# Optimization experiments

Measured on AMD Instinct MI355X. Metric: run time of the kernel, lower is better.

The kernel has to match this reference:

```python
import jax, jax.numpy as jnp
import numpy as np

B, S, D = 2, 2048, 1024
H, DH = 16, 64
IGNORE = -100000.0
ATTN_SCALE = float(np.sqrt(DH))


def setup_inputs() -> dict:
    key = jax.random.key(0)
    ks = jax.random.split(key, 9)
    sc = 0.02
    return {
        "x": jax.random.normal(ks[0], (B, S, D), dtype=jnp.float32),
        "W_Q": jax.random.normal(ks[1], (H, DH, D), dtype=jnp.float32) * sc,
        "W_K": jax.random.normal(ks[2], (H, DH, D), dtype=jnp.float32) * sc,
        "W_V": jax.random.normal(ks[3], (H, DH, D), dtype=jnp.float32) * sc,
        "W_O": jax.random.normal(ks[4], (H, D, DH), dtype=jnp.float32) * sc,
        "b_Q": jax.random.normal(ks[5], (H, DH), dtype=jnp.float32) * sc,
        "b_K": jax.random.normal(ks[6], (H, DH), dtype=jnp.float32) * sc,
        "b_V": jax.random.normal(ks[7], (H, DH), dtype=jnp.float32) * sc,
        "b_O": jax.random.normal(ks[8], (D,), dtype=jnp.float32) * sc,
    }


def reference(x, W_Q, W_K, W_V, W_O, b_Q, b_K, b_V, b_O):
    # QKV projections: [b, pos, head, d_head]
    q = jnp.einsum('ihm,bpm->bpih', W_Q, x) + b_Q
    k = jnp.einsum('ihm,bpm->bpih', W_K, x) + b_K
    v = jnp.einsum('ihm,bpm->bpih', W_V, x) + b_V
    # scores[b, head, query_pos, key_pos]
    scores = jnp.einsum('bpih,bqih->bipq', q, k) / ATTN_SCALE
    Sq = x.shape[1]
    causal = jnp.tril(jnp.ones((Sq, Sq), dtype=bool))  # global causal mask
    scores = jnp.where(causal, scores, jnp.float32(IGNORE))
    attn = jax.nn.softmax(scores, axis=-1)
    # z[b, query_pos, head, d_head]
    z = jnp.einsum('bpih,biqp->bqih', v, attn)
    out = jnp.einsum('idh,bqih->bqd', W_O, z) + b_O
    return out
```

## Files before the change

kernel.cpp:

```cpp
#include <hip/hip_runtime.h>
#include <stdint.h>

typedef __attribute__((ext_vector_type(8))) short short8;
typedef __attribute__((ext_vector_type(4))) float f32x4;

#define AS1(p) ((const __attribute__((address_space(1))) void*)(p))
#define AS3(p) ((__attribute__((address_space(3))) void*)(p))

__device__ __forceinline__ void gload_lds16(const void* g, void* l) {
  __builtin_amdgcn_global_load_lds(AS1(g), AS3(l), 16, 0, 0);
}

__device__ __forceinline__ uint32_t cvtpk_bf16(float a, float b) {
  uint32_t d;
  asm("v_cvt_pk_bf16_f32 %0, %1, %2" : "=v"(d) : "v"(a), "v"(b));
  return d;
}

__device__ __forceinline__ float fast_exp2(float x) {
#if __has_builtin(__builtin_amdgcn_exp2f)
  return __builtin_amdgcn_exp2f(x);
#else
  return exp2f(x);
#endif
}

#define QSCALE 0.1803368801111244f

__global__ void prep_k(const float* __restrict__ x, const float* __restrict__ wq,
                       const float* __restrict__ wk, const float* __restrict__ wv,
                       const float* __restrict__ wo, const float* __restrict__ bq,
                       const float* __restrict__ bk, const float* __restrict__ bv,
                       uint2* __restrict__ xb, uint2* __restrict__ wqkvb,
                       uint2* __restrict__ mob, float* __restrict__ bqkv) {
  const int bid = blockIdx.x, tid = threadIdx.x;
  if (bid < 4096) {
    int i = bid * 256 + tid;
    float4 v = ((const float4*)x)[i];
    uint2 o; o.x = cvtpk_bf16(v.x, v.y); o.y = cvtpk_bf16(v.z, v.w);
    xb[i] = o;
  } else if (bid < 7168) {
    int i = (bid - 4096) * 256 + tid;
    int e = i * 4;
    const float* src = (e < (1 << 20)) ? (wq + e)
                     : (e < (2 << 20)) ? (wk + (e - (1 << 20)))
                                       : (wv + (e - (2 << 20)));
    float4 v = *(const float4*)src;
    uint2 o; o.x = cvtpk_bf16(v.x, v.y); o.y = cvtpk_bf16(v.z, v.w);
    wqkvb[i] = o;
  } else if (bid < 8192) {
    int i = (bid - 7168) * 256 + tid;
    int o4 = i * 4;
    int d = o4 >> 10, c = o4 & 1023;
    const float* s = wo + ((c >> 6) << 16) + (d << 6) + (c & 63);
    float4 v = *(const float4*)s;
    uint2 o; o.x = cvtpk_bf16(v.x, v.y); o.y = cvtpk_bf16(v.z, v.w);
    mob[i] = o;
  } else {
    int i = (bid - 8192) * 256 + tid;
    bqkv[i] = (i < 1024) ? bq[i] : (i < 2048) ? bk[i - 1024] : bv[i - 2048];
  }
}

__global__ __launch_bounds__(256) void gemm_bt(const short* __restrict__ A,
                                               const short* __restrict__ Bm,
                                               const float* __restrict__ bias,
                                               unsigned short* __restrict__ Cout,
                                               int K, int ldc) {
  __shared__ short As[128 * 64];
  __shared__ short Bs[128 * 64];
  const int t = threadIdx.x;
  const int l = t & 63, w = t >> 6;
  const int wr = w >> 1, wc = w & 1;
  const int q = l & 15, g = l >> 4;
  const long brow = (long)blockIdx.y * 128;
  const long bcol = (long)blockIdx.x * 128;
  f32x4 acc[4][4] = {};
  const int r8 = t >> 3;
  const int sc8 = (t & 7) ^ (r8 & 7);
  const short* aptr = A + (brow + r8) * (long)K + sc8 * 8;
  const short* bptr = Bm + (bcol + r8) * (long)K + sc8 * 8;
  const int qs = q & 7;
  for (int k0 = 0; k0 < K; k0 += 64) {
#pragma unroll
    for (int c = 0; c < 4; ++c) {
      gload_lds16(aptr + k0 + c * 32 * (long)K, &As[(c * 256 + t) * 8]);
      gload_lds16(bptr + k0 + c * 32 * (long)K, &Bs[(c * 256 + t) * 8]);
    }
    __syncthreads();
    short8 af[4][2], bfr[4][2];
#pragma unroll
    for (int m = 0; m < 4; ++m)
#pragma unroll
      for (int kk = 0; kk < 2; ++kk)
        af[m][kk] = *(const short8*)&As[(wr * 64 + m * 16 + q) * 64 + ((kk * 4 + g) ^ qs) * 8];
#pragma unroll
    for (int n = 0; n < 4; ++n)
#pragma unroll
      for (int kk = 0; kk < 2; ++kk)
        bfr[n][kk] = *(const short8*)&Bs[(wc * 64 + n * 16 + q) * 64 + ((kk * 4 + g) ^ qs) * 8];
#pragma unroll
    for (int m = 0; m < 4; ++m)
#pragma unroll
      for (int n = 0; n < 4; ++n) {
        acc[m][n] = __builtin_amdgcn_mfma_f32_16x16x32_bf16(af[m][0], bfr[n][0], acc[m][n], 0, 0, 0);
        acc[m][n] = __builtin_amdgcn_mfma_f32_16x16x32_bf16(af[m][1], bfr[n][1], acc[m][n], 0, 0, 0);
      }
    if (k0 + 64 < K) __syncthreads();
  }
#pragma unroll
  for (int m = 0; m < 4; ++m)
#pragma unroll
    for (int n = 0; n < 4; ++n)
#pragma unroll
      for (int r = 0; r < 4; ++r) {
        long row = brow + wr * 64 + m * 16 + g * 4 + r;
        long col = bcol + wc * 64 + n * 16 + q;
        float v = acc[m][n][r] + bias[col];
        if (col < 1024) v *= QSCALE;
        Cout[row * ldc + col] = (unsigned short)cvtpk_bf16(v, v);
      }
}

__global__ __launch_bounds__(256) void gemm_bt2(const short* __restrict__ A,
                                                const short* __restrict__ Bm,
                                                const float* __restrict__ bias,
                                                float* __restrict__ Cout,
                                                int K, int ldc) {
  __shared__ short As[128 * 64];
  __shared__ short Bs[64 * 64];
  const int t = threadIdx.x;
  const int l = t & 63, w = t >> 6;
  const int q = l & 15, g = l >> 4;
  const long brow = (long)blockIdx.y * 128;
  const long bcol = (long)blockIdx.x * 64;
  f32x4 acc[2][4] = {};
  const int r8 = t >> 3;
  const int sc8 = (t & 7) ^ (r8 & 7);
  const short* aptr = A + (brow + r8) * (long)K + sc8 * 8;
  const short* bptr = Bm + (bcol + r8) * (long)K + sc8 * 8;
  const int qs = q & 7;
  for (int k0 = 0; k0 < K; k0 += 64) {
#pragma unroll
    for (int c = 0; c < 4; ++c)
      gload_lds16(aptr + k0 + c * 32 * (long)K, &As[(c * 256 + t) * 8]);
#pragma unroll
    for (int c = 0; c < 2; ++c)
      gload_lds16(bptr + k0 + c * 32 * (long)K, &Bs[(c * 256 + t) * 8]);
    __syncthreads();
    short8 af[2][2], bfr[4][2];
#pragma unroll
    for (int m = 0; m < 2; ++m)
#pragma unroll
      for (int kk = 0; kk < 2; ++kk)
        af[m][kk] = *(const short8*)&As[(w * 32 + m * 16 + q) * 64 + ((kk * 4 + g) ^ qs) * 8];
#pragma unroll
    for (int n = 0; n < 4; ++n)
#pragma unroll
      for (int kk = 0; kk < 2; ++kk)
        bfr[n][kk] = *(const short8*)&Bs[(n * 16 + q) * 64 + ((kk * 4 + g) ^ qs) * 8];
#pragma unroll
    for (int m = 0; m < 2; ++m)
#pragma unroll
      for (int n = 0; n < 4; ++n) {
        acc[m][n] = __builtin_amdgcn_mfma_f32_16x16x32_bf16(af[m][0], bfr[n][0], acc[m][n], 0, 0, 0);
        acc[m][n] = __builtin_amdgcn_mfma_f32_16x16x32_bf16(af[m][1], bfr[n][1], acc[m][n], 0, 0, 0);
      }
    if (k0 + 64 < K) __syncthreads();
  }
#pragma unroll
  for (int m = 0; m < 2; ++m)
#pragma unroll
    for (int n = 0; n < 4; ++n)
#pragma unroll
      for (int r = 0; r < 4; ++r) {
        long row = brow + w * 32 + m * 16 + g * 4 + r;
        long col = bcol + n * 16 + q;
        Cout[row * ldc + col] = acc[m][n][r] + bias[col];
      }
}

__global__ __launch_bounds__(256) void attn(const short* __restrict__ qkv,
                                            unsigned short* __restrict__ zb) {
  __shared__ short Ks[2][64 * 64];
  __shared__ short Vt[64 * 64];
  __shared__ unsigned short Ps[8][16 * 64];
  const int bid = blockIdx.x;
  const int r_ = bid >> 7;
  const int u_ = (bid >> 3) & 15;
  const int x_ = bid & 7;
  const int bh = r_ * 8 + x_;
  const int pr = (r_ < 2) ? u_ : 15 - u_;
  const int qtA = 31 - pr, qtB = pr;
  const int b = bh >> 4, h = bh & 15;
  const int t = threadIdx.x, l = t & 63, w = t >> 6;
  const int lq = l & 15, g = l >> 4;
  const int u = t >> 3, c8 = t & 7;
  const long rowbase = (long)b * 2048;
  const short* qp = qkv + rowbase * 3072 + h * 64;
  const short* kp = qp + 1024;
  const short* vp = qp + 2048;

  short8 qfA[2], qfB[2];
#pragma unroll
  for (int kg = 0; kg < 2; ++kg) {
    qfA[kg] = *(const short8*)(qp + (long)(qtA * 64 + w * 16 + lq) * 3072 + kg * 32 + g * 8);
    qfB[kg] = *(const short8*)(qp + (long)(qtB * 64 + w * 16 + lq) * 3072 + kg * 32 + g * 8);
  }
  f32x4 zA[4] = {}, zB[4] = {};
  float mA = -1e30f, lA = 0.0f, mB = -1e30f, lB = 0.0f;

  auto step = [&](const short* ksb, unsigned short* Pw, f32x4 (&zacc)[4],
                  float& mrun, float& lrun, short8 (&qf)[2], bool diag) {
    f32x4 sacc[4] = {};
#pragma unroll
    for (int m = 0; m < 4; ++m) {
#pragma unroll
      for (int kg = 0; kg < 2; ++kg) {
        int krow = m * 16 + lq;
        int blk = kg * 4 + g;
        short8 kf = *(const short8*)&ksb[krow * 64 + (blk ^ (krow & 7)) * 8];
        sacc[m] = __builtin_amdgcn_mfma_f32_16x16x32_bf16(kf, qf[kg], sacc[m], 0, 0, 0);
      }
    }
    if (diag) {
#pragma unroll
      for (int m = 0; m < 4; ++m)
#pragma unroll
        for (int r = 0; r < 4; ++r)
          if (m * 16 + g * 4 + r > w * 16 + lq) sacc[m][r] = -1e30f;
    }
    float red[8];
#pragma unroll
    for (int i2 = 0; i2 < 8; ++i2)
      red[i2] = fmaxf(sacc[i2 >> 2][i2 & 3], sacc[2 + (i2 >> 2)][i2 & 3]);
#pragma unroll
    for (int i2 = 0; i2 < 4; ++i2) red[i2] = fmaxf(red[i2], red[i2 + 4]);
    float mx = fmaxf(fmaxf(red[0], red[2]), fmaxf(red[1], red[3]));
    mx = fmaxf(mx, __shfl_xor(mx, 16));
    mx = fmaxf(mx, __shfl_xor(mx, 32));
    if (!__all(mx <= mrun + 8.0f)) {
      float mnew = fmaxf(mrun, mx);
      float alpha = fast_exp2(mrun - mnew);
      lrun *= alpha;
#pragma unroll
      for (int r = 0; r < 4; ++r) {
        float ar = __shfl(alpha, g * 4 + r);
#pragma unroll
        for (int n2 = 0; n2 < 4; ++n2) zacc[n2][r] *= ar;
      }
      mrun = mnew;
    }
#pragma unroll
    for (int m = 0; m < 4; ++m)
#pragma unroll
      for (int r = 0; r < 4; ++r) sacc[m][r] = fast_exp2(sacc[m][r] - mrun);
    float rs[8];
#pragma unroll
    for (int i2 = 0; i2 < 8; ++i2)
      rs[i2] = sacc[i2 >> 2][i2 & 3] + sacc[2 + (i2 >> 2)][i2 & 3];
#pragma unroll
    for (int i2 = 0; i2 < 4; ++i2) rs[i2] = rs[i2] + rs[i2 + 4];
    float ts = (rs[0] + rs[2]) + (rs[1] + rs[3]);
    ts += __shfl_xor(ts, 16);
    ts += __shfl_xor(ts, 32);
    lrun += ts;
#pragma unroll
    for (int m = 0; m < 4; ++m) {
      uint2 wv;
      wv.x = cvtpk_bf16(sacc[m][0], sacc[m][1]);
      wv.y = cvtpk_bf16(sacc[m][2], sacc[m][3]);
      int c = m * 4 + g;
      int csw = c ^ ((lq & 7) << 1);
      *(uint2*)&Pw[lq * 64 + csw * 4] = wv;
    }
    short8 pf[2];
#pragma unroll
    for (int kg2 = 0; kg2 < 2; ++kg2) {
      int c0 = kg2 * 8 + g * 2;
      int c0s = c0 ^ ((lq & 7) << 1);
      pf[kg2] = *(const short8*)&Pw[lq * 64 + c0s * 4];
    }
#pragma unroll
    for (int n2 = 0; n2 < 4; ++n2) {
#pragma unroll
      for (int kg2 = 0; kg2 < 2; ++kg2) {
        int dh = n2 * 16 + lq;
        int sw = (dh & 7) ^ ((dh >> 3) & 7);
        int blk = kg2 * 4 + g;
        short8 vf = *(const short8*)&Vt[dh * 64 + ((blk ^ sw) * 8)];
        zacc[n2] = __builtin_amdgcn_mfma_f32_16x16x32_bf16(pf[kg2], vf, zacc[n2], 0, 0, 0);
      }
    }
  };

  auto stageK = [&](int tile, int buf) {
#pragma unroll
    for (int i = 0; i < 2; ++i) {
      int r = i * 32 + u;
      int cbk = (c8 ^ (r & 7)) * 8;
      gload_lds16(kp + (long)(tile * 64 + r) * 3072 + cbk, &Ks[buf][i * 2048 + t * 8]);
    }
  };

  short8 va0, va1;
  {
    stageK(0, 0);
    const short* vrow = vp + (long)(2 * u) * 3072 + c8 * 8;
    va0 = *(const short8*)vrow;
    va1 = *(const short8*)(vrow + 3072);
  }

  for (int j = 0; j <= qtA; ++j) {
    const int buf = j & 1;
    asm volatile("s_waitcnt vmcnt(0)" ::: "memory");
    __builtin_amdgcn_sched_barrier(0);
    __builtin_amdgcn_s_barrier();
    {
      int blk = u >> 2, rl = (u & 3) * 2;
#pragma unroll
      for (int idx = 0; idx < 8; ++idx) {
        int dh = c8 * 8 + idx;
        int sw = (dh & 7) ^ ((dh >> 3) & 7);
        uint32_t pk = (uint32_t)(uint16_t)va0[idx] | ((uint32_t)(uint16_t)va1[idx] << 16);
        *(uint32_t*)&Vt[dh * 64 + ((blk ^ sw) * 8) + rl] = pk;
      }
    }
    if (j < qtA) {
      stageK(j + 1, buf ^ 1);
      const short* vrow = vp + (long)((j + 1) * 64 + 2 * u) * 3072 + c8 * 8;
      va0 = *(const short8*)vrow;
      va1 = *(const short8*)(vrow + 3072);
    }
    asm volatile("s_waitcnt lgkmcnt(0)" ::: "memory");
    __builtin_amdgcn_sched_barrier(0);
    __builtin_amdgcn_s_barrier();
    step(&Ks[buf][0], &Ps[w][0], zA, mA, lA, qfA, j == qtA);
    if (j <= qtB)
      step(&Ks[buf][0], &Ps[4 + w][0], zB, mB, lB, qfB, j == qtB);
  }

  auto wout = [&](f32x4 (&zacc)[4], float lrun, int qt) {
#pragma unroll
    for (int r = 0; r < 4; ++r) {
      float linv = 1.0f / __shfl(lrun, g * 4 + r);
      long grow = rowbase + qt * 64 + w * 16 + g * 4 + r;
#pragma unroll
      for (int n2 = 0; n2 < 4; ++n2) {
        int col = h * 64 + n2 * 16 + lq;
        float zv = zacc[n2][r] * linv;
        zb[grow * 1024 + col] = (unsigned short)cvtpk_bf16(zv, zv);
      }
    }
  };
  wout(zA, lA, qtA);
  wout(zB, lB, qtB);
}

extern "C" void kernel_launch(void* const* d_in, const int* in_sizes, int n_in,
                              void* d_out, int out_size, void* d_ws, size_t ws_size,
                              hipStream_t stream) {
  const float* x  = (const float*)d_in[0];
  const float* wq = (const float*)d_in[1];
  const float* wk = (const float*)d_in[2];
  const float* wv = (const float*)d_in[3];
  const float* wo = (const float*)d_in[4];
  const float* bq = (const float*)d_in[5];
  const float* bk = (const float*)d_in[6];
  const float* bv = (const float*)d_in[7];
  const float* bo = (const float*)d_in[8];
  char* ws = (char*)d_ws;
  if (ws_size < ((size_t)48 * 1024 * 1024 + 16384)) return;
  short*          xb    = (short*)(ws);
  short*          qkvb  = (short*)(ws + ((size_t)8  << 20));
  unsigned short* zbuf  = (unsigned short*)(ws + ((size_t)32 << 20));
  short*          wqkvb = (short*)(ws + ((size_t)40 << 20));
  short*          mob   = (short*)(ws + ((size_t)46 << 20));
  float*          bqkv  = (float*)(ws + ((size_t)48 << 20));

  prep_k<<<8204, 256, 0, stream>>>(x, wq, wk, wv, wo, bq, bk, bv,
                                   (uint2*)xb, (uint2*)wqkvb, (uint2*)mob, bqkv);
  gemm_bt <<<dim3(24, 32), 256, 0, stream>>>(xb, wqkvb, bqkv, (unsigned short*)qkvb, 1024, 3072);
  attn    <<<512,          256, 0, stream>>>(qkvb, zbuf);
  gemm_bt2<<<dim3(16, 32), 256, 0, stream>>>((const short*)zbuf, mob, bo, (float*)d_out, 1024, 1024);
}
```

Before: 106.9 us.

## Double-buffer LDS tiles in projection GEMMs with BK=32 prefetch

Both the QKV and output projection GEMMs move from a single 64-wide K tile to two 32-wide LDS buffers. The next tile is issued with global_load_lds while MFMAs run on the current one, with a new XOR swizzle for the 4-chunk rows. The aim is to hide global load latency behind compute. In exchange there are twice as many loop iterations and barriers, and less MFMA work per barrier.

```diff
diff --git a/kernel.cpp b/kernel.cpp
--- a/kernel.cpp
+++ b/kernel.cpp
@@ -67,8 +67,8 @@
                                                const float* __restrict__ bias,
                                                unsigned short* __restrict__ Cout,
                                                int K, int ldc) {
-  __shared__ short As[128 * 64];
-  __shared__ short Bs[128 * 64];
+  __shared__ short As[2][128 * 32];
+  __shared__ short Bs[2][128 * 32];
   const int t = threadIdx.x;
   const int l = t & 63, w = t >> 6;
   const int wr = w >> 1, wc = w & 1;
@@ -76,37 +76,40 @@
   const long brow = (long)blockIdx.y * 128;
   const long bcol = (long)blockIdx.x * 128;
   f32x4 acc[4][4] = {};
-  const int r8 = t >> 3;
-  const int sc8 = (t & 7) ^ (r8 & 7);
-  const short* aptr = A + (brow + r8) * (long)K + sc8 * 8;
-  const short* bptr = Bm + (bcol + r8) * (long)K + sc8 * 8;
-  const int qs = q & 7;
-  for (int k0 = 0; k0 < K; k0 += 64) {
-#pragma unroll
-    for (int c = 0; c < 4; ++c) {
-      gload_lds16(aptr + k0 + c * 32 * (long)K, &As[(c * 256 + t) * 8]);
-      gload_lds16(bptr + k0 + c * 32 * (long)K, &Bs[(c * 256 + t) * 8]);
-    }
+  const int r4 = t >> 2;
+  const int sc4 = (t & 3) ^ ((r4 >> 1) & 3);
+  const short* aptr = A + (brow + r4) * (long)K + sc4 * 8;
+  const short* bptr = Bm + (bcol + r4) * (long)K + sc4 * 8;
+  auto stage = [&](int k0, int buf) {
+#pragma unroll
+    for (int p = 0; p < 2; ++p) {
+      gload_lds16(aptr + k0 + (long)p * 64 * K, &As[buf][(p * 256 + t) * 8]);
+      gload_lds16(bptr + k0 + (long)p * 64 * K, &Bs[buf][(p * 256 + t) * 8]);
+    }
+  };
+  stage(0, 0);
+  __syncthreads();
+  int cur = 0;
+  for (int k0 = 0; k0 < K; k0 += 32) {
+    if (k0 + 32 < K) stage(k0 + 32, cur ^ 1);
+    short8 af[4], bfr[4];
+#pragma unroll
+    for (int m = 0; m < 4; ++m) {
+      int row = wr * 64 + m * 16 + q;
+      af[m] = *(const short8*)&As[cur][(row * 4 + (g ^ ((row >> 1) & 3))) * 8];
+    }
+#pragma unroll
+    for (int n = 0; n < 4; ++n) {
+      int row = wc * 64 + n * 16 + q;
+      bfr[n] = *(const short8*)&Bs[cur][(row * 4 + (g ^ ((row >> 1) & 3))) * 8];
+    }
+#pragma unroll
+    for (int m = 0; m < 4; ++m)
+#pragma unroll
+      for (int n = 0; n < 4; ++n)
+        acc[m][n] = __builtin_amdgcn_mfma_f32_16x16x32_bf16(af[m], bfr[n], acc[m][n], 0, 0, 0);
     __syncthreads();
-    short8 af[4][2], bfr[4][2];
-#pragma unroll
-    for (int m = 0; m < 4; ++m)
-#pragma unroll
-      for (int kk = 0; kk < 2; ++kk)
-        af[m][kk] = *(const short8*)&As[(wr * 64 + m * 16 + q) * 64 + ((kk * 4 + g) ^ qs) * 8];
-#pragma unroll
-    for (int n = 0; n < 4; ++n)
-#pragma unroll
-      for (int kk = 0; kk < 2; ++kk)
-        bfr[n][kk] = *(const short8*)&Bs[(wc * 64 + n * 16 + q) * 64 + ((kk * 4 + g) ^ qs) * 8];
-#pragma unroll
-    for (int m = 0; m < 4; ++m)
-#pragma unroll
-      for (int n = 0; n < 4; ++n) {
-        acc[m][n] = __builtin_amdgcn_mfma_f32_16x16x32_bf16(af[m][0], bfr[n][0], acc[m][n], 0, 0, 0);
-        acc[m][n] = __builtin_amdgcn_mfma_f32_16x16x32_bf16(af[m][1], bfr[n][1], acc[m][n], 0, 0, 0);
-      }
-    if (k0 + 64 < K) __syncthreads();
+    cur ^= 1;
   }
 #pragma unroll
   for (int m = 0; m < 4; ++m)
@@ -127,46 +130,46 @@
                                                 const float* __restrict__ bias,
                                                 float* __restrict__ Cout,
                                                 int K, int ldc) {
-  __shared__ short As[128 * 64];
-  __shared__ short Bs[64 * 64];
+  __shared__ short As[2][128 * 32];
+  __shared__ short Bs[2][64 * 32];
   const int t = threadIdx.x;
   const int l = t & 63, w = t >> 6;
   const int q = l & 15, g = l >> 4;
   const long brow = (long)blockIdx.y * 128;
   const long bcol = (long)blockIdx.x * 64;
   f32x4 acc[2][4] = {};
-  const int r8 = t >> 3;
-  const int sc8 = (t & 7) ^ (r8 & 7);
-  const short* aptr = A + (brow + r8) * (long)K + sc8 * 8;
-  const short* bptr = Bm + (bcol + r8) * (long)K + sc8 * 8;
-  const int qs = q & 7;
-  for (int k0 = 0; k0 < K; k0 += 64) {
-#pragma unroll
-    for (int c = 0; c < 4; ++c)
-      gload_lds16(aptr + k0 + c * 32 * (long)K, &As[(c * 256 + t) * 8]);
-#pragma unroll
-    for (int c = 0; c < 2; ++c)
-      gload_lds16(bptr + k0 + c * 32 * (long)K, &Bs[(c * 256 + t) * 8]);
+  const int r4 = t >> 2;
+  const int sc4 = (t & 3) ^ ((r4 >> 1) & 3);
+  const short* aptr = A + (brow + r4) * (long)K + sc4 * 8;
+  const short* bptr = Bm + (bcol + r4) * (long)K + sc4 * 8;
+  auto stage = [&](int k0, int buf) {
+    gload_lds16(aptr + k0, &As[buf][t * 8]);
+    gload_lds16(aptr + k0 + (long)64 * K, &As[buf][(256 + t) * 8]);
+    gload_lds16(bptr + k0, &Bs[buf][t * 8]);
+  };
+  stage(0, 0);
+  __syncthreads();
+  int cur = 0;
+  for (int k0 = 0; k0 < K; k0 += 32) {
+    if (k0 + 32 < K) stage(k0 + 32, cur ^ 1);
+    short8 af[2], bfr[4];
+#pragma unroll
+    for (int m = 0; m < 2; ++m) {
+      int row = w * 32 + m * 16 + q;
+      af[m] = *(const short8*)&As[cur][(row * 4 + (g ^ ((row >> 1) & 3))) * 8];
+    }
+#pragma unroll
+    for (int n = 0; n < 4; ++n) {
+      int row = n * 16 + q;
+      bfr[n] = *(const short8*)&Bs[cur][(row * 4 + (g ^ ((row >> 1) & 3))) * 8];
+    }
+#pragma unroll
+    for (int m = 0; m < 2; ++m)
+#pragma unroll
+      for (int n = 0; n < 4; ++n)
+        acc[m][n] = __builtin_amdgcn_mfma_f32_16x16x32_bf16(af[m], bfr[n], acc[m][n], 0, 0, 0);
     __syncthreads();
-    short8 af[2][2], bfr[4][2];
-#pragma unroll
-    for (int m = 0; m < 2; ++m)
-#pragma unroll
-      for (int kk = 0; kk < 2; ++kk)
-        af[m][kk] = *(const short8*)&As[(w * 32 + m * 16 + q) * 64 + ((kk * 4 + g) ^ qs) * 8];
-#pragma unroll
-    for (int n = 0; n < 4; ++n)
-#pragma unroll
-      for (int kk = 0; kk < 2; ++kk)
-        bfr[n][kk] = *(const short8*)&Bs[(n * 16 + q) * 64 + ((kk * 4 + g) ^ qs) * 8];
-#pragma unroll
-    for (int m = 0; m < 2; ++m)
-#pragma unroll
-      for (int n = 0; n < 4; ++n) {
-        acc[m][n] = __builtin_amdgcn_mfma_f32_16x16x32_bf16(af[m][0], bfr[n][0], acc[m][n], 0, 0, 0);
-        acc[m][n] = __builtin_amdgcn_mfma_f32_16x16x32_bf16(af[m][1], bfr[n][1], acc[m][n], 0, 0, 0);
-      }
-    if (k0 + 64 < K) __syncthreads();
+    cur ^= 1;
   }
 #pragma unroll
   for (int m = 0; m < 2; ++m)
```

Result: slower. 115.2 us (+7.8%).
